# Kernel tuning notes

Measured on AMD Instinct MI355X. Metric: run time of the kernel, lower is better.

## Reference

```python
import jax, jax.numpy as jnp
import numpy as np

N = 100000   # nodes
E = 1600000  # edges
G = 256      # graphs in batch
F_IN = 64
H = 64
C = 10


def setup_inputs() -> dict:
    key = jax.random.key(0)
    ks = jax.random.split(key, 16)
    x = jax.random.normal(ks[0], (N, F_IN), dtype=jnp.float32)
    edge_index = jax.random.randint(ks[1], (2, E), 0, N, dtype=jnp.int32)
    batch = jnp.sort(jax.random.randint(ks[2], (N,), 0, G, dtype=jnp.int32))
    def lin(k, i, o):
        return jax.random.normal(k, (i, o), dtype=jnp.float32) / np.sqrt(i).astype(np.float32)
    return {
        'x': x, 'edge_index': edge_index, 'batch': batch,
        'W1': lin(ks[3], F_IN, H), 'b1': jnp.zeros((H,), jnp.float32),
        'W2': lin(ks[4], H, H),    'b2': jnp.zeros((H,), jnp.float32),
        'W3': lin(ks[5], H, H),    'b3': jnp.zeros((H,), jnp.float32),
        'fc1_w': lin(ks[6], 3 * H, H),      'fc1_b': jnp.zeros((H,), jnp.float32),
        'fc2_w': lin(ks[7], H, H // 2),     'fc2_b': jnp.zeros((H // 2,), jnp.float32),
        'fc3_w': lin(ks[8], H // 2, C),     'fc3_b': jnp.zeros((C,), jnp.float32),
    }


def _gcn_layer(h_in, W, b, src, dst, deg_inv_sqrt):
    # GCNConv: h = X W ; out = D^-1/2 (A + I) D^-1/2 h + b ; then ReLU
    h = h_in @ W
    norm = deg_inv_sqrt[src] * deg_inv_sqrt[dst]            # [E]
    agg = jax.ops.segment_sum(h[src] * norm[:, None], dst, num_segments=N)
    agg = agg + h * (deg_inv_sqrt * deg_inv_sqrt)[:, None]  # self-loop term
    return jax.nn.relu(agg + b)


def _pool(h, batch):
    # concat(mean, max, add) pooling by graph id
    s = jax.ops.segment_sum(h, batch, num_segments=G)
    cnt = jax.ops.segment_sum(jnp.ones((h.shape[0], 1), h.dtype), batch, num_segments=G)
    mean = s / jnp.maximum(cnt, 1.0)
    mx = jnp.maximum(jax.ops.segment_max(h, batch, num_segments=G), 0.0)  # h >= 0 post-ReLU
    return jnp.concatenate([mean, mx, s], axis=1)  # [G, 3H]


def reference(x, edge_index, batch, W1, b1, W2, b2, W3, b3,
              fc1_w, fc1_b, fc2_w, fc2_b, fc3_w, fc3_b):
    src, dst = edge_index[0], edge_index[1]
    # degree including self loop (edge weight 1)
    deg = jax.ops.segment_sum(jnp.ones((E,), x.dtype), dst, num_segments=N) + 1.0
    dis = jax.lax.rsqrt(deg)

    h1 = _gcn_layer(x, W1, b1, src, dst, dis)
    p1 = _pool(h1, batch)
    h2 = _gcn_layer(h1, W2, b2, src, dst, dis)
    p2 = _pool(h2, batch)
    h3 = _gcn_layer(h2, W3, b3, src, dst, dis)
    p3 = _pool(h3, batch)

    z = p1 + p2 + p3                              # [G, 3H]
    z = jax.nn.relu(z @ fc1_w + fc1_b)            # dropout inactive (eval)
    z = jax.nn.relu(z @ fc2_w + fc2_b)
    return jax.nn.log_softmax(z @ fc3_w + fc3_b, axis=-1)
```

## Files before the change

### kernel.cpp

```cpp
#include <hip/hip_runtime.h>
#include <cmath>

typedef unsigned int uint;
typedef __attribute__((ext_vector_type(8))) short short8;
typedef __attribute__((ext_vector_type(4))) float f32x4;
typedef __attribute__((ext_vector_type(4))) int i32x4;

__device__ inline float bflo(uint u) { return __uint_as_float(u << 16); }
__device__ inline float bfhi(uint u) { return __uint_as_float(u & 0xffff0000u); }
__device__ inline ushort bf1(float a) {
  uint ua = __float_as_uint(a);
  return (ushort)((ua + 0x7fffu + ((ua >> 16) & 1u)) >> 16);
}
__device__ inline uint bfpack(float a, float b) {
  uint ua = __float_as_uint(a), ub = __float_as_uint(b);
  uint ra = (ua + 0x7fffu + ((ua >> 16) & 1u)) >> 16;
  uint rb = (ub + 0x7fffu + ((ub >> 16) & 1u)) >> 16;
  return ra | (rb << 16);
}

#define SLOT_CAP 48
#define FILL_CHUNK 4096
#define BSHIFT 8
#define NPB 256
#define MAXB 512
#define BCAP 5120
#define PSPLIT 4

__global__ __launch_bounds__(256) void prep_k(const float* __restrict__ W1, const float* __restrict__ W2,
                                              const float* __restrict__ W3,
                                              ushort* __restrict__ T1, ushort* __restrict__ T2,
                                              ushort* __restrict__ T3,
                                              const int* __restrict__ batch, int* __restrict__ gstart,
                                              int* __restrict__ bcnt, ushort* __restrict__ hlin,
                                              float* __restrict__ zpool, int zcount,
                                              int n, int G, int bnd) {
  int b = blockIdx.x;
  int t = threadIdx.x;
  if (b < 48) {
    int sel = b >> 4;
    int i = (b & 15) * 256 + t;
    const float* W = (sel == 0) ? W1 : (sel == 1) ? W2 : W3;
    ushort* T = (sel == 0) ? T1 : (sel == 1) ? T2 : T3;
    int c = i >> 6, k = i & 63;
    T[i] = bf1(W[k * 64 + c]);
  } else if (b < 48 + bnd) {
    int i = (b - 48) * 256 + t;
    if (i >= n) return;
    int bb = batch[i];
    int prev = (i == 0) ? -1 : batch[i - 1];
    for (int g = prev + 1; g <= bb; ++g) gstart[g] = i;
    if (i == n - 1) { for (int g = bb + 1; g <= G; ++g) gstart[g] = n; }
  } else if (b == 48 + bnd) {
    if (t < 32) ((uint*)(hlin + (size_t)n * 64))[t] = 0u;
    bcnt[t] = 0; bcnt[t + 256] = 0;
  } else {
    int idx = (b - 49 - bnd) * 256 + t;
    if (idx < zcount) zpool[idx] = 0.f;
  }
}

__global__ __launch_bounds__(256) void part_k(const int* __restrict__ src, const int* __restrict__ dst,
                                              int* __restrict__ bcnt, uint* __restrict__ buckets,
                                              int E, int nb) {
  __shared__ int lcnt[MAXB], lbase[MAXB];
  int t = threadIdx.x;
  for (int i = t; i < nb; i += 256) lcnt[i] = 0;
  __syncthreads();
  int base = blockIdx.x * FILL_CHUNK;
  int d[16];
  #pragma unroll
  for (int i = 0; i < 16; ++i) {
    int e = base + t + i * 256;
    d[i] = (e < E) ? __builtin_nontemporal_load(dst + e) : -1;
    if (d[i] >= 0) atomicAdd(&lcnt[d[i] >> BSHIFT], 1);
  }
  __syncthreads();
  for (int i = t; i < nb; i += 256) { lbase[i] = atomicAdd(&bcnt[i], lcnt[i]); lcnt[i] = 0; }
  __syncthreads();
  #pragma unroll
  for (int i = 0; i < 16; ++i) {
    if (d[i] >= 0) {
      int e = base + t + i * 256;
      int r = d[i] >> BSHIFT;
      int rank = atomicAdd(&lcnt[r], 1);
      uint s = (uint)__builtin_nontemporal_load(src + e);
      uint packed = (s << 8) | (uint)(d[i] & (NPB - 1));
      buckets[(size_t)r * BCAP + lbase[r] + rank] = packed;
    }
  }
}

__global__ __launch_bounds__(256) void fillB_k(const uint* __restrict__ buckets,
                                               const int* __restrict__ bcnt,
                                               int* __restrict__ cursor, int* __restrict__ csr,
                                               float* __restrict__ dis,
                                               int nb, int N) {
  __shared__ int lcnt[NPB];
  __shared__ int rows[NPB][SLOT_CAP];
  int r = blockIdx.x;
  int t = threadIdx.x;
  if (t < NPB) lcnt[t] = 0;
  i32x4* rinit = (i32x4*)&rows[0][0];
  for (int i = t; i < NPB * SLOT_CAP / 4; i += 256) rinit[i] = (i32x4){N, N, N, N};
  __syncthreads();
  int n = bcnt[r];
  const uint* bk = buckets + (size_t)r * BCAP;
  for (int i = t; i < n; i += 256) {
    uint e = __builtin_nontemporal_load(&bk[i]);
    int dl = (int)(e & (NPB - 1));
    int s = (int)(e >> 8);
    int pos = atomicAdd(&lcnt[dl], 1);
    if (pos < SLOT_CAP) rows[dl][pos] = s;
  }
  __syncthreads();
  int base_node = r << BSHIFT;
  int nodes_here = N - base_node; if (nodes_here > NPB) nodes_here = NPB;
  if (nodes_here <= 0) return;
  int total4 = nodes_here * (SLOT_CAP / 4);
  i32x4* dstp = (i32x4*)(csr + (size_t)base_node * SLOT_CAP);
  const i32x4* srcp = (const i32x4*)&rows[0][0];
  for (int i = t; i < total4; i += 256) dstp[i] = srcp[i];
  for (int i = t; i < nodes_here; i += 256) {
    int c = lcnt[i];
    cursor[base_node + i] = c;
    dis[base_node + i] = rsqrtf((float)c + 1.0f);
  }
}

__global__ __launch_bounds__(256) void gemm_mfma_k(const ushort* __restrict__ X,
                                                   const float* __restrict__ Xf,
                                                   const ushort* __restrict__ WT,
                                                   const float* __restrict__ dis,
                                                   ushort* __restrict__ Y, int n) {
  int t = threadIdx.x;
  int wv = t >> 6, lane = t & 63;
  int m = lane & 15, quad = lane >> 4;
  int row = blockIdx.x * 64 + wv * 16 + m;
  int rclamp = (row < n) ? row : 0;
  short8 a0, a1;
  if (Xf) {
    const float4* af = (const float4*)(Xf + (size_t)rclamp * 64);
    float4 v0 = af[quad * 2],     v1 = af[quad * 2 + 1];
    float4 v2 = af[quad * 2 + 8], v3 = af[quad * 2 + 9];
    union { uint u[4]; short8 s; } c0, c1;
    c0.u[0] = bfpack(v0.x, v0.y); c0.u[1] = bfpack(v0.z, v0.w);
    c0.u[2] = bfpack(v1.x, v1.y); c0.u[3] = bfpack(v1.z, v1.w);
    c1.u[0] = bfpack(v2.x, v2.y); c1.u[1] = bfpack(v2.z, v2.w);
    c1.u[2] = bfpack(v3.x, v3.y); c1.u[3] = bfpack(v3.z, v3.w);
    a0 = c0.s; a1 = c1.s;
  } else {
    const short8* arow = (const short8*)(X + (size_t)rclamp * 64);
    a0 = arow[quad];
    a1 = arow[quad + 4];
  }
  f32x4 acc[4];
  #pragma unroll
  for (int ct = 0; ct < 4; ++ct) {
    const short8* wrow = (const short8*)(WT + (size_t)(ct * 16 + m) * 64);
    short8 b0 = wrow[quad];
    short8 b1 = wrow[quad + 4];
    f32x4 a = {0.f, 0.f, 0.f, 0.f};
    a = __builtin_amdgcn_mfma_f32_16x16x32_bf16(a0, b0, a, 0, 0, 0);
    a = __builtin_amdgcn_mfma_f32_16x16x32_bf16(a1, b1, a, 0, 0, 0);
    acc[ct] = a;
  }
  int orow = blockIdx.x * 64 + wv * 16 + quad * 4;
  #pragma unroll
  for (int reg = 0; reg < 4; ++reg) {
    int r = orow + reg;
    if (r < n) {
      float ds = dis[r];
      #pragma unroll
      for (int ct = 0; ct < 4; ++ct)
        Y[(size_t)r * 64 + ct * 16 + m] = bf1(acc[ct][reg] * ds);
    }
  }
}

__global__ __launch_bounds__(256) void agg_k(const ushort* __restrict__ Hs,
                                             const int* __restrict__ csr,
                                             const int* __restrict__ cnt,
                                             const float* __restrict__ dis,
                                             const float* __restrict__ bias,
                                             ushort* __restrict__ Hout, int n) {
  int wv = __builtin_amdgcn_readfirstlane((int)(threadIdx.x >> 6));
  int lane = threadIdx.x & 63;
  int node = blockIdx.x * 4 + wv;
  if (node >= n) return;
  float dn = dis[node];
  int deg = __builtin_nontemporal_load(cnt + node);
  if (deg > SLOT_CAP) deg = SLOT_CAP;
  const i32x4* rp = (const i32x4*)(csr + (size_t)node * SLOT_CAP);
  float acc = bflo((uint)Hs[(size_t)node * 64 + lane]);

  i32x4 r0 = __builtin_nontemporal_load(rp + 0);
  i32x4 r1 = __builtin_nontemporal_load(rp + 1);
  i32x4 r2 = __builtin_nontemporal_load(rp + 2);
  i32x4 r3 = __builtin_nontemporal_load(rp + 3);
  i32x4 r4 = __builtin_nontemporal_load(rp + 4);
  i32x4 r5 = __builtin_nontemporal_load(rp + 5);
  i32x4 r6 = __builtin_nontemporal_load(rp + 6);
  i32x4 r7 = __builtin_nontemporal_load(rp + 7);
  int sa[32] = {r0.x, r0.y, r0.z, r0.w, r1.x, r1.y, r1.z, r1.w,
                r2.x, r2.y, r2.z, r2.w, r3.x, r3.y, r3.z, r3.w,
                r4.x, r4.y, r4.z, r4.w, r5.x, r5.y, r5.z, r5.w,
                r6.x, r6.y, r6.z, r6.w, r7.x, r7.y, r7.z, r7.w};
  float ha[32];
  #pragma unroll
  for (int i = 0; i < 32; ++i) ha[i] = bflo((uint)Hs[(size_t)sa[i] * 64 + lane]);
  #pragma unroll
  for (int i = 0; i < 32; ++i) acc += ha[i];

  if (deg > 32) {
    i32x4 r8  = __builtin_nontemporal_load(rp + 8);
    i32x4 r9  = __builtin_nontemporal_load(rp + 9);
    i32x4 r10 = __builtin_nontemporal_load(rp + 10);
    i32x4 r11 = __builtin_nontemporal_load(rp + 11);
    int sb[16] = {r8.x, r8.y, r8.z, r8.w, r9.x, r9.y, r9.z, r9.w,
                  r10.x, r10.y, r10.z, r10.w, r11.x, r11.y, r11.z, r11.w};
    float hb[16];
    #pragma unroll
    for (int i = 0; i < 16; ++i) hb[i] = bflo((uint)Hs[(size_t)sb[i] * 64 + lane]);
    #pragma unroll
    for (int i = 0; i < 16; ++i) acc += hb[i];
  }

  float v = fmaxf(fmaf(dn, acc, bias[lane]), 0.f);
  Hout[(size_t)node * 64 + lane] = bf1(v);
}

__global__ __launch_bounds__(256) void pool_k(const ushort* __restrict__ H, const int* __restrict__ gstart,
                                              float* __restrict__ zsum, uint* __restrict__ zmax) {
  int g = blockIdx.x / PSPLIT;
  int q = blockIdx.x % PSPLIT;
  int t = threadIdx.x;
  int lane = t & 63, w = t >> 6;
  int slot = lane >> 3, fl = lane & 7;
  int i0 = gstart[g], i1 = gstart[g + 1];
  float s[8], m[8];
  #pragma unroll
  for (int j = 0; j < 8; ++j) { s[j] = 0.f; m[j] = 0.f; }
  for (int i = i0 + q * 32 + w * 8 + slot; i < i1; i += 32 * PSPLIT) {
    uint4 v = ((const uint4*)(H + (size_t)i * 64))[fl];
    float f[8] = { bflo(v.x), bfhi(v.x), bflo(v.y), bfhi(v.y),
                   bflo(v.z), bfhi(v.z), bflo(v.w), bfhi(v.w) };
    #pragma unroll
    for (int j = 0; j < 8; ++j) { s[j] += f[j]; m[j] = fmaxf(m[j], f[j]); }
  }
  #pragma unroll
  for (int msk = 8; msk <= 32; msk <<= 1) {
    #pragma unroll
    for (int j = 0; j < 8; ++j) {
      s[j] += __shfl_xor(s[j], msk, 64);
      m[j] = fmaxf(m[j], __shfl_xor(m[j], msk, 64));
    }
  }
  __shared__ float ss[4][64], sm[4][64];
  if (slot == 0) {
    #pragma unroll
    for (int j = 0; j < 8; ++j) { ss[w][fl * 8 + j] = s[j]; sm[w][fl * 8 + j] = m[j]; }
  }
  __syncthreads();
  if (t < 64) {
    float S = (ss[0][t] + ss[1][t]) + (ss[2][t] + ss[3][t]);
    float M = fmaxf(fmaxf(sm[0][t], sm[1][t]), fmaxf(sm[2][t], sm[3][t]));
    atomicAdd(&zsum[g * 64 + t], S);
    atomicMax(&zmax[g * 64 + t], __float_as_uint(M));
  }
}

__global__ __launch_bounds__(64) void mlp_k(const float* __restrict__ zsum,
                                            const uint* __restrict__ zmax, int G64,
                                            const int* __restrict__ gstart,
                                            const float* __restrict__ fc1w, const float* __restrict__ fc1b,
                                            const float* __restrict__ fc2w, const float* __restrict__ fc2b,
                                            const float* __restrict__ fc3w, const float* __restrict__ fc3b,
                                            float* __restrict__ out) {
  int g = blockIdx.x; int t = threadIdx.x;
  __shared__ float zr[192], a1[64], a2[32], a3[10];
  float S = zsum[g * 64 + t];
  float M = __uint_as_float(zmax[g * 64 + t])
          + __uint_as_float(zmax[G64 + g * 64 + t])
          + __uint_as_float(zmax[2 * G64 + g * 64 + t]);
  float cntf = (float)(gstart[g + 1] - gstart[g]);
  zr[t]       = (cntf > 0.f) ? S / cntf : 0.f;
  zr[64 + t]  = M;
  zr[128 + t] = S;
  __syncthreads();
  float acc = fc1b[t];
  for (int k = 0; k < 192; ++k) acc += zr[k] * fc1w[k * 64 + t];
  a1[t] = fmaxf(acc, 0.f);
  __syncthreads();
  if (t < 32) {
    float a = fc2b[t];
    #pragma unroll
    for (int k = 0; k < 64; ++k) a += a1[k] * fc2w[k * 32 + t];
    a2[t] = fmaxf(a, 0.f);
  }
  __syncthreads();
  if (t < 10) {
    float a = fc3b[t];
    #pragma unroll
    for (int k = 0; k < 32; ++k) a += a2[k] * fc3w[k * 10 + t];
    a3[t] = a;
  }
  __syncthreads();
  if (t == 0) {
    float mx = a3[0];
    for (int i = 1; i < 10; ++i) mx = fmaxf(mx, a3[i]);
    float sum = 0.f;
    for (int i = 0; i < 10; ++i) sum += expf(a3[i] - mx);
    float lse = mx + logf(sum);
    for (int i = 0; i < 10; ++i) out[g * 10 + i] = a3[i] - lse;
  }
}

extern "C" void kernel_launch(void* const* d_in, const int* in_sizes, int n_in,
                              void* d_out, int out_size, void* d_ws, size_t ws_size,
                              hipStream_t stream) {
  const float* x    = (const float*)d_in[0];
  const int*   ei   = (const int*)  d_in[1];
  const int*   batch= (const int*)  d_in[2];
  const float* W1   = (const float*)d_in[3];
  const float* b1   = (const float*)d_in[4];
  const float* W2   = (const float*)d_in[5];
  const float* b2   = (const float*)d_in[6];
  const float* W3   = (const float*)d_in[7];
  const float* b3   = (const float*)d_in[8];
  const float* fc1w = (const float*)d_in[9];
  const float* fc1b = (const float*)d_in[10];
  const float* fc2w = (const float*)d_in[11];
  const float* fc2b = (const float*)d_in[12];
  const float* fc3w = (const float*)d_in[13];
  const float* fc3b = (const float*)d_in[14];
  float* out = (float*)d_out;

  const int N = in_sizes[0] / 64;
  const int E = in_sizes[1] / 2;
  const int G = out_size / 10;
  const int* src = ei;
  const int* dst = ei + E;
  const int nb = (N + NPB - 1) >> BSHIFT;

  char* p = (char*)d_ws;
  auto alloc = [&](size_t bytes) -> void* {
    void* r = (void*)p; p += (bytes + 255) & ~(size_t)255; return r;
  };
  int*       cursor  = (int*)      alloc((size_t)N * 4);
  int*       bcnt    = (int*)      alloc(MAXB * 4);
  float*     dis     = (float*)    alloc((size_t)N * 4);
  int*       gstart  = (int*)      alloc((size_t)(G + 1) * 4);
  int*       csr     = (int*)      alloc((size_t)(nb * NPB) * SLOT_CAP * 4);
  uint*      buckets = (uint*)     alloc((size_t)nb * BCAP * 4);
  ushort*    wt1     = (ushort*)   alloc(4096 * 2);
  ushort*    wt2     = (ushort*)   alloc(4096 * 2);
  ushort*    wt3     = (ushort*)   alloc(4096 * 2);
  ushort*    hlin    = (ushort*)   alloc((size_t)(N + 1) * 64 * 2);
  ushort*    hA      = (ushort*)   alloc((size_t)N * 64 * 2);
  float*     zpool   = (float*)    alloc((size_t)4 * G * 64 * 4);
  float*     zsum    = zpool;
  uint*      zmax    = (uint*)(zpool + (size_t)G * 64);
  (void)ws_size; (void)n_in;

  int G64 = G * 64;
  int bnd = (N + 255) >> 8;
  int zcount = 4 * G64;
  int prep_grid = 48 + bnd + 1 + (zcount + 255) / 256;
  prep_k<<<prep_grid, 256, 0, stream>>>(W1, W2, W3, wt1, wt2, wt3, batch, gstart,
                                        bcnt, hlin, zpool, zcount, N, G, bnd);
  int chunks = (E + FILL_CHUNK - 1) / FILL_CHUNK;
  part_k<<<chunks, 256, 0, stream>>>(src, dst, bcnt, buckets, E, nb);
  fillB_k<<<nb, 256, 0, stream>>>(buckets, bcnt, cursor, csr, dis, nb, N);

  int gb = (N + 63) / 64;
  int ab = (N + 3) / 4;
  gemm_mfma_k<<<gb, 256, 0, stream>>>(nullptr, x, wt1, dis, hlin, N);
  agg_k<<<ab, 256, 0, stream>>>(hlin, csr, cursor, dis, b1, hA, N);
  pool_k<<<G * PSPLIT, 256, 0, stream>>>(hA, gstart, zsum, zmax + 0 * G64);
  gemm_mfma_k<<<gb, 256, 0, stream>>>(hA, nullptr, wt2, dis, hlin, N);
  agg_k<<<ab, 256, 0, stream>>>(hlin, csr, cursor, dis, b2, hA, N);
  pool_k<<<G * PSPLIT, 256, 0, stream>>>(hA, gstart, zsum, zmax + 1 * G64);
  gemm_mfma_k<<<gb, 256, 0, stream>>>(hA, nullptr, wt3, dis, hlin, N);
  agg_k<<<ab, 256, 0, stream>>>(hlin, csr, cursor, dis, b3, hA, N);
  pool_k<<<G * PSPLIT, 256, 0, stream>>>(hA, gstart, zsum, zmax + 2 * G64);

  mlp_k<<<G, 64, 0, stream>>>(zsum, zmax, G64, gstart, fc1w, fc1b, fc2w, fc2b, fc3w, fc3b, out);
}
```

Before: 302.8 us.

## Aggregate before transform and fuse pooling into the GEMM epilogue

Reorders each GCN layer to aggregate first, (A+I)·D^-1/2·X, and then multiply by W, which is valid because the layer is linear. The GEMM epilogue now applies bias and ReLU, writes the dis-scaled input for the next layer, and does per-block sum/max pooling with atomics. This removes the three separate pool kernels and their full re-read of the hidden activations. It adds one small cast kernel for x, and assumes each 64-row block spans at most two graphs.

```diff
diff --git a/kernel.cpp b/kernel.cpp
--- a/kernel.cpp
+++ b/kernel.cpp
@@ -25,14 +25,13 @@
 #define NPB 256
 #define MAXB 512
 #define BCAP 5120
-#define PSPLIT 4
 
 __global__ __launch_bounds__(256) void prep_k(const float* __restrict__ W1, const float* __restrict__ W2,
                                               const float* __restrict__ W3,
                                               ushort* __restrict__ T1, ushort* __restrict__ T2,
                                               ushort* __restrict__ T3,
                                               const int* __restrict__ batch, int* __restrict__ gstart,
-                                              int* __restrict__ bcnt, ushort* __restrict__ hlin,
+                                              int* __restrict__ bcnt, ushort* __restrict__ sbuf,
                                               float* __restrict__ zpool, int zcount,
                                               int n, int G, int bnd) {
   int b = blockIdx.x;
@@ -52,7 +51,7 @@
     for (int g = prev + 1; g <= bb; ++g) gstart[g] = i;
     if (i == n - 1) { for (int g = bb + 1; g <= G; ++g) gstart[g] = n; }
   } else if (b == 48 + bnd) {
-    if (t < 32) ((uint*)(hlin + (size_t)n * 64))[t] = 0u;
+    if (t < 32) ((uint*)(sbuf + (size_t)n * 64))[t] = 0u;
     bcnt[t] = 0; bcnt[t + 256] = 0;
   } else {
     int idx = (b - 49 - bnd) * 256 + t;
@@ -128,62 +127,20 @@
   }
 }
 
-__global__ __launch_bounds__(256) void gemm_mfma_k(const ushort* __restrict__ X,
-                                                   const float* __restrict__ Xf,
-                                                   const ushort* __restrict__ WT,
-                                                   const float* __restrict__ dis,
-                                                   ushort* __restrict__ Y, int n) {
-  int t = threadIdx.x;
-  int wv = t >> 6, lane = t & 63;
-  int m = lane & 15, quad = lane >> 4;
-  int row = blockIdx.x * 64 + wv * 16 + m;
-  int rclamp = (row < n) ? row : 0;
-  short8 a0, a1;
-  if (Xf) {
-    const float4* af = (const float4*)(Xf + (size_t)rclamp * 64);
-    float4 v0 = af[quad * 2],     v1 = af[quad * 2 + 1];
-    float4 v2 = af[quad * 2 + 8], v3 = af[quad * 2 + 9];
-    union { uint u[4]; short8 s; } c0, c1;
-    c0.u[0] = bfpack(v0.x, v0.y); c0.u[1] = bfpack(v0.z, v0.w);
-    c0.u[2] = bfpack(v1.x, v1.y); c0.u[3] = bfpack(v1.z, v1.w);
-    c1.u[0] = bfpack(v2.x, v2.y); c1.u[1] = bfpack(v2.z, v2.w);
-    c1.u[2] = bfpack(v3.x, v3.y); c1.u[3] = bfpack(v3.z, v3.w);
-    a0 = c0.s; a1 = c1.s;
-  } else {
-    const short8* arow = (const short8*)(X + (size_t)rclamp * 64);
-    a0 = arow[quad];
-    a1 = arow[quad + 4];
-  }
-  f32x4 acc[4];
-  #pragma unroll
-  for (int ct = 0; ct < 4; ++ct) {
-    const short8* wrow = (const short8*)(WT + (size_t)(ct * 16 + m) * 64);
-    short8 b0 = wrow[quad];
-    short8 b1 = wrow[quad + 4];
-    f32x4 a = {0.f, 0.f, 0.f, 0.f};
-    a = __builtin_amdgcn_mfma_f32_16x16x32_bf16(a0, b0, a, 0, 0, 0);
-    a = __builtin_amdgcn_mfma_f32_16x16x32_bf16(a1, b1, a, 0, 0, 0);
-    acc[ct] = a;
-  }
-  int orow = blockIdx.x * 64 + wv * 16 + quad * 4;
-  #pragma unroll
-  for (int reg = 0; reg < 4; ++reg) {
-    int r = orow + reg;
-    if (r < n) {
-      float ds = dis[r];
-      #pragma unroll
-      for (int ct = 0; ct < 4; ++ct)
-        Y[(size_t)r * 64 + ct * 16 + m] = bf1(acc[ct][reg] * ds);
-    }
-  }
-}
-
-__global__ __launch_bounds__(256) void agg_k(const ushort* __restrict__ Hs,
+__global__ __launch_bounds__(256) void xcast_k(const float* __restrict__ X, const float* __restrict__ dis,
+                                               ushort* __restrict__ S, int total4) {
+  int i = blockIdx.x * 256 + threadIdx.x;
+  if (i >= total4) return;
+  float ds = dis[i >> 4];
+  float4 v = ((const float4*)X)[i];
+  ((uint2*)S)[i] = make_uint2(bfpack(v.x * ds, v.y * ds), bfpack(v.z * ds, v.w * ds));
+}
+
+__global__ __launch_bounds__(256) void agg_k(const ushort* __restrict__ S,
                                              const int* __restrict__ csr,
                                              const int* __restrict__ cnt,
                                              const float* __restrict__ dis,
-                                             const float* __restrict__ bias,
-                                             ushort* __restrict__ Hout, int n) {
+                                             ushort* __restrict__ P, int n) {
   int wv = __builtin_amdgcn_readfirstlane((int)(threadIdx.x >> 6));
   int lane = threadIdx.x & 63;
   int node = blockIdx.x * 4 + wv;
@@ -192,7 +149,7 @@
   int deg = __builtin_nontemporal_load(cnt + node);
   if (deg > SLOT_CAP) deg = SLOT_CAP;
   const i32x4* rp = (const i32x4*)(csr + (size_t)node * SLOT_CAP);
-  float acc = bflo((uint)Hs[(size_t)node * 64 + lane]);
+  float acc = bflo((uint)S[(size_t)node * 64 + lane]);
 
   i32x4 r0 = __builtin_nontemporal_load(rp + 0);
   i32x4 r1 = __builtin_nontemporal_load(rp + 1);
@@ -208,7 +165,7 @@
                 r6.x, r6.y, r6.z, r6.w, r7.x, r7.y, r7.z, r7.w};
   float ha[32];
   #pragma unroll
-  for (int i = 0; i < 32; ++i) ha[i] = bflo((uint)Hs[(size_t)sa[i] * 64 + lane]);
+  for (int i = 0; i < 32; ++i) ha[i] = bflo((uint)S[(size_t)sa[i] * 64 + lane]);
   #pragma unroll
   for (int i = 0; i < 32; ++i) acc += ha[i];
 
@@ -221,52 +178,93 @@
                   r10.x, r10.y, r10.z, r10.w, r11.x, r11.y, r11.z, r11.w};
     float hb[16];
     #pragma unroll
-    for (int i = 0; i < 16; ++i) hb[i] = bflo((uint)Hs[(size_t)sb[i] * 64 + lane]);
+    for (int i = 0; i < 16; ++i) hb[i] = bflo((uint)S[(size_t)sb[i] * 64 + lane]);
     #pragma unroll
     for (int i = 0; i < 16; ++i) acc += hb[i];
   }
 
-  float v = fmaxf(fmaf(dn, acc, bias[lane]), 0.f);
-  Hout[(size_t)node * 64 + lane] = bf1(v);
-}
-
-__global__ __launch_bounds__(256) void pool_k(const ushort* __restrict__ H, const int* __restrict__ gstart,
-                                              float* __restrict__ zsum, uint* __restrict__ zmax) {
-  int g = blockIdx.x / PSPLIT;
-  int q = blockIdx.x % PSPLIT;
+  P[(size_t)node * 64 + lane] = bf1(dn * acc);
+}
+
+__global__ __launch_bounds__(256) void gemmP_k(const ushort* __restrict__ P,
+                                               const ushort* __restrict__ WT,
+                                               const float* __restrict__ dis,
+                                               const float* __restrict__ bias,
+                                               const int* __restrict__ batch,
+                                               ushort* __restrict__ Sout,
+                                               float* __restrict__ zsum, uint* __restrict__ zmax,
+                                               int n) {
   int t = threadIdx.x;
-  int lane = t & 63, w = t >> 6;
-  int slot = lane >> 3, fl = lane & 7;
-  int i0 = gstart[g], i1 = gstart[g + 1];
-  float s[8], m[8];
-  #pragma unroll
-  for (int j = 0; j < 8; ++j) { s[j] = 0.f; m[j] = 0.f; }
-  for (int i = i0 + q * 32 + w * 8 + slot; i < i1; i += 32 * PSPLIT) {
-    uint4 v = ((const uint4*)(H + (size_t)i * 64))[fl];
-    float f[8] = { bflo(v.x), bfhi(v.x), bflo(v.y), bfhi(v.y),
-                   bflo(v.z), bfhi(v.z), bflo(v.w), bfhi(v.w) };
-    #pragma unroll
-    for (int j = 0; j < 8; ++j) { s[j] += f[j]; m[j] = fmaxf(m[j], f[j]); }
-  }
-  #pragma unroll
-  for (int msk = 8; msk <= 32; msk <<= 1) {
-    #pragma unroll
-    for (int j = 0; j < 8; ++j) {
-      s[j] += __shfl_xor(s[j], msk, 64);
-      m[j] = fmaxf(m[j], __shfl_xor(m[j], msk, 64));
-    }
-  }
-  __shared__ float ss[4][64], sm[4][64];
-  if (slot == 0) {
-    #pragma unroll
-    for (int j = 0; j < 8; ++j) { ss[w][fl * 8 + j] = s[j]; sm[w][fl * 8 + j] = m[j]; }
+  int wv = t >> 6, lane = t & 63;
+  int m = lane & 15, quad = lane >> 4;
+  int row = blockIdx.x * 64 + wv * 16 + m;
+  int rclamp = (row < n) ? row : 0;
+  const short8* arow = (const short8*)(P + (size_t)rclamp * 64);
+  short8 a0 = arow[quad];
+  short8 a1 = arow[quad + 4];
+  f32x4 acc[4];
+  #pragma unroll
+  for (int ct = 0; ct < 4; ++ct) {
+    const short8* wrow = (const short8*)(WT + (size_t)(ct * 16 + m) * 64);
+    short8 b0 = wrow[quad];
+    short8 b1 = wrow[quad + 4];
+    f32x4 a = {0.f, 0.f, 0.f, 0.f};
+    a = __builtin_amdgcn_mfma_f32_16x16x32_bf16(a0, b0, a, 0, 0, 0);
+    a = __builtin_amdgcn_mfma_f32_16x16x32_bf16(a1, b1, a, 0, 0, 0);
+    acc[ct] = a;
+  }
+  int blockRow = blockIdx.x * 64;
+  int g0 = batch[blockRow];
+  int rl = blockRow + 63; if (rl > n - 1) rl = n - 1;
+  int gl = batch[rl];
+  int orow = blockRow + wv * 16 + quad * 4;
+  float s0a[4] = {0.f, 0.f, 0.f, 0.f}, s1a[4] = {0.f, 0.f, 0.f, 0.f};
+  float m0a[4] = {0.f, 0.f, 0.f, 0.f}, m1a[4] = {0.f, 0.f, 0.f, 0.f};
+  #pragma unroll
+  for (int reg = 0; reg < 4; ++reg) {
+    int r = orow + reg;
+    bool valid = (r < n);
+    int gr = valid ? batch[r] : g0;
+    bool to1 = (gr != g0);
+    float ds = valid ? dis[r] : 0.f;
+    #pragma unroll
+    for (int ct = 0; ct < 4; ++ct) {
+      float h = valid ? fmaxf(acc[ct][reg] + bias[ct * 16 + m], 0.f) : 0.f;
+      if (Sout && valid) Sout[(size_t)r * 64 + ct * 16 + m] = bf1(h * ds);
+      if (to1) { s1a[ct] += h; m1a[ct] = fmaxf(m1a[ct], h); }
+      else     { s0a[ct] += h; m0a[ct] = fmaxf(m0a[ct], h); }
+    }
+  }
+  #pragma unroll
+  for (int msk = 16; msk <= 32; msk <<= 1) {
+    #pragma unroll
+    for (int ct = 0; ct < 4; ++ct) {
+      s0a[ct] += __shfl_xor(s0a[ct], msk, 64);
+      s1a[ct] += __shfl_xor(s1a[ct], msk, 64);
+      m0a[ct] = fmaxf(m0a[ct], __shfl_xor(m0a[ct], msk, 64));
+      m1a[ct] = fmaxf(m1a[ct], __shfl_xor(m1a[ct], msk, 64));
+    }
+  }
+  __shared__ float ls0[4][64], ls1[4][64], lm0[4][64], lm1[4][64];
+  if (quad == 0) {
+    #pragma unroll
+    for (int ct = 0; ct < 4; ++ct) {
+      ls0[wv][ct * 16 + m] = s0a[ct]; ls1[wv][ct * 16 + m] = s1a[ct];
+      lm0[wv][ct * 16 + m] = m0a[ct]; lm1[wv][ct * 16 + m] = m1a[ct];
+    }
   }
   __syncthreads();
   if (t < 64) {
-    float S = (ss[0][t] + ss[1][t]) + (ss[2][t] + ss[3][t]);
-    float M = fmaxf(fmaxf(sm[0][t], sm[1][t]), fmaxf(sm[2][t], sm[3][t]));
-    atomicAdd(&zsum[g * 64 + t], S);
-    atomicMax(&zmax[g * 64 + t], __float_as_uint(M));
+    float S0 = (ls0[0][t] + ls0[1][t]) + (ls0[2][t] + ls0[3][t]);
+    float M0 = fmaxf(fmaxf(lm0[0][t], lm0[1][t]), fmaxf(lm0[2][t], lm0[3][t]));
+    atomicAdd(&zsum[g0 * 64 + t], S0);
+    atomicMax(&zmax[g0 * 64 + t], __float_as_uint(M0));
+    if (gl != g0) {
+      float S1 = (ls1[0][t] + ls1[1][t]) + (ls1[2][t] + ls1[3][t]);
+      float M1 = fmaxf(fmaxf(lm1[0][t], lm1[1][t]), fmaxf(lm1[2][t], lm1[3][t]));
+      atomicAdd(&zsum[gl * 64 + t], S1);
+      atomicMax(&zmax[gl * 64 + t], __float_as_uint(M1));
+    }
   }
 }
 
@@ -356,8 +354,8 @@
   ushort*    wt1     = (ushort*)   alloc(4096 * 2);
   ushort*    wt2     = (ushort*)   alloc(4096 * 2);
   ushort*    wt3     = (ushort*)   alloc(4096 * 2);
-  ushort*    hlin    = (ushort*)   alloc((size_t)(N + 1) * 64 * 2);
-  ushort*    hA      = (ushort*)   alloc((size_t)N * 64 * 2);
+  ushort*    sbuf    = (ushort*)   alloc((size_t)(N + 1) * 64 * 2);
+  ushort*    pbuf    = (ushort*)   alloc((size_t)N * 64 * 2);
   float*     zpool   = (float*)    alloc((size_t)4 * G * 64 * 4);
   float*     zsum    = zpool;
   uint*      zmax    = (uint*)(zpool + (size_t)G * 64);
@@ -368,22 +366,20 @@
   int zcount = 4 * G64;
   int prep_grid = 48 + bnd + 1 + (zcount + 255) / 256;
   prep_k<<<prep_grid, 256, 0, stream>>>(W1, W2, W3, wt1, wt2, wt3, batch, gstart,
-                                        bcnt, hlin, zpool, zcount, N, G, bnd);
+                                        bcnt, sbuf, zpool, zcount, N, G, bnd);
   int chunks = (E + FILL_CHUNK - 1) / FILL_CHUNK;
   part_k<<<chunks, 256, 0, stream>>>(src, dst, bcnt, buckets, E, nb);
   fillB_k<<<nb, 256, 0, stream>>>(buckets, bcnt, cursor, csr, dis, nb, N);
+  xcast_k<<<(N * 16 + 255) / 256, 256, 0, stream>>>(x, dis, sbuf, N * 16);
 
   int gb = (N + 63) / 64;
   int ab = (N + 3) / 4;
-  gemm_mfma_k<<<gb, 256, 0, stream>>>(nullptr, x, wt1, dis, hlin, N);
-  agg_k<<<ab, 256, 0, stream>>>(hlin, csr, cursor, dis, b1, hA, N);
-  pool_k<<<G * PSPLIT, 256, 0, stream>>>(hA, gstart, zsum, zmax + 0 * G64);
-  gemm_mfma_k<<<gb, 256, 0, stream>>>(hA, nullptr, wt2, dis, hlin, N);
-  agg_k<<<ab, 256, 0, stream>>>(hlin, csr, cursor, dis, b2, hA, N);
-  pool_k<<<G * PSPLIT, 256, 0, stream>>>(hA, gstart, zsum, zmax + 1 * G64);
-  gemm_mfma_k<<<gb, 256, 0, stream>>>(hA, nullptr, wt3, dis, hlin, N);
-  agg_k<<<ab, 256, 0, stream>>>(hlin, csr, cursor, dis, b3, hA, N);
-  pool_k<<<G * PSPLIT, 256, 0, stream>>>(hA, gstart, zsum, zmax + 2 * G64);
+  agg_k<<<ab, 256, 0, stream>>>(sbuf, csr, cursor, dis, pbuf, N);
+  gemmP_k<<<gb, 256, 0, stream>>>(pbuf, wt1, dis, b1, batch, sbuf, zsum, zmax + 0 * G64, N);
+  agg_k<<<ab, 256, 0, stream>>>(sbuf, csr, cursor, dis, pbuf, N);
+  gemmP_k<<<gb, 256, 0, stream>>>(pbuf, wt2, dis, b2, batch, sbuf, zsum, zmax + 1 * G64, N);
+  agg_k<<<ab, 256, 0, stream>>>(sbuf, csr, cursor, dis, pbuf, N);
+  gemmP_k<<<gb, 256, 0, stream>>>(pbuf, wt3, dis, b3, batch, nullptr, zsum, zmax + 2 * G64, N);
 
   mlp_k<<<G, 64, 0, stream>>>(zsum, zmax, G64, gstart, fc1w, fc1b, fc2w, fc2b, fc3w, fc3b, out);
 }
```

New measurement: 299.7 us. About the same (-1.0%).
